# Optimization experiments

Hardware: AMD Instinct MI355X
Metric: run time of the kernel (lower is better)

The kernel has to match this reference:

```python
import math
import jax, jax.numpy as jnp
import numpy as np

DIM = 512
HEADS = 8
B, N = 4, 2048


def _linear_params(key, d_in, d_out):
    # torch nn.Linear default init: U(-1/sqrt(d_in), 1/sqrt(d_in))
    k1, k2 = jax.random.split(key)
    bound = 1.0 / math.sqrt(d_in)
    W = jax.random.uniform(k1, (d_out, d_in), minval=-bound, maxval=bound, dtype=jnp.float32)
    b = jax.random.uniform(k2, (d_out,), minval=-bound, maxval=bound, dtype=jnp.float32)
    return W, b


def setup_inputs() -> dict:
    key = jax.random.key(0)
    kq, kv, km, k1, k2, k3, k4 = jax.random.split(key, 7)
    Q = jax.random.normal(kq, (B, N, DIM), dtype=jnp.float32)
    V = jax.random.normal(kv, (B, N, DIM), dtype=jnp.float32)
    mask = jax.random.bernoulli(km, 0.9, (B, N))  # bool [B, Nk]
    Wq, bq = _linear_params(k1, DIM, DIM)
    Wk, bk = _linear_params(k2, DIM, DIM)
    Wv, bv = _linear_params(k3, DIM, DIM)
    Wo, bo = _linear_params(k4, DIM, DIM)
    return {"Q": Q, "V": V, "mask": mask,
            "Wq": Wq, "bq": bq, "Wk": Wk, "bk": bk,
            "Wv": Wv, "bv": bv, "Wo": Wo, "bo": bo}


def reference(Q, V, mask, Wq, bq, Wk, bk, Wv, bv, Wo, bo):
    Bb, Nq, _ = Q.shape
    dv = Wq.shape[0]
    h = HEADS
    d = dv // h
    q = Q @ Wq.T + bq          # [B, Nq, dv]
    k = V @ Wk.T + bk          # [B, Nk, dv]
    v = V @ Wv.T + bv          # [B, Nk, dv]
    # split heads: torch.cat(split(dim_split, dim=2), dim=0) == head-major stacking
    qh = q.reshape(Bb, Nq, h, d).transpose(2, 0, 1, 3)   # [h, B, Nq, d]
    kh = k.reshape(Bb, -1, h, d).transpose(2, 0, 1, 3)   # [h, B, Nk, d]
    vh = v.reshape(Bb, -1, h, d).transpose(2, 0, 1, 3)   # [h, B, Nk, d]
    # NOTE: original scales by sqrt(Q.shape[-1]) AFTER projection == sqrt(dim_V)
    logits = jnp.einsum('hbqd,hbkd->hbqk', qh, kh) / math.sqrt(dv)
    logits = jnp.where(mask[None, :, None, :], logits, jnp.float32(-100.0))
    A = jax.nn.softmax(logits, axis=-1)
    Oh = qh + jnp.einsum('hbqk,hbkd->hbqd', A, vh)       # residual inside attention
    O = Oh.transpose(1, 2, 0, 3).reshape(Bb, Nq, dv)     # merge heads
    return O + jax.nn.relu(O @ Wo.T + bo)
```

## Files before the change

kernel.cpp:

```cpp
#include <hip/hip_runtime.h>


typedef __attribute__((ext_vector_type(8))) __bf16 bf16x8;
typedef __attribute__((ext_vector_type(4))) float f32x4;

#define DEV static __device__ __forceinline__

constexpr int DIMC = 512;
constexpr int NTOK = 2048;
constexpr int BB   = 4;
constexpr int MTOK = BB * NTOK;
constexpr float SCALE2 = 0.04419417382415922f * 1.4426950408889634f;

DEV unsigned short f2b(float f) {
  unsigned u = __float_as_uint(f);
  u = (u + 0x7FFFu + ((u >> 16) & 1u)) >> 16;
  return (unsigned short)u;
}
DEV float b2f(unsigned short b) { return __uint_as_float(((unsigned)b) << 16); }

DEV unsigned cvtpk(float a, float b) {
  unsigned r;
  asm("v_cvt_pk_bf16_f32 %0, %1, %2" : "=v"(r) : "v"(a), "v"(b));
  return r;
}

DEV bf16x8 pack8(unsigned d0, unsigned d1, unsigned d2, unsigned d3) {
  union { unsigned u[4]; bf16x8 v; } t;
  t.u[0] = d0; t.u[1] = d1; t.u[2] = d2; t.u[3] = d3;
  return t.v;
}

DEV void async_cp16(const void* src, void* dst) {
  __builtin_amdgcn_global_load_lds(
      (const __attribute__((address_space(1))) void*)(src),
      (__attribute__((address_space(3))) void*)(dst), 16, 0, 0);
}

__global__ __launch_bounds__(256) void proj_gemm(
    const float* __restrict__ Qf, const float* __restrict__ Vf,
    const float* __restrict__ Wq, const float* __restrict__ Wk,
    const float* __restrict__ Wv,
    const float* __restrict__ bq, const float* __restrict__ bk,
    const float* __restrict__ bv,
    unsigned short* __restrict__ qbf, unsigned short* __restrict__ kbf,
    unsigned short* __restrict__ vtb,
    const unsigned char* __restrict__ mask, int* __restrict__ flag) {
  __shared__ union {
    struct { float A[2][4096]; float B[2][4096]; } s;
    unsigned short LT[128 * 136];
  } lds;

  const int region = blockIdx.z;
  const float* Af = (region == 0) ? Qf : Vf;
  const float* W = (region == 0) ? Wq : (region == 1) ? Wk : Wv;
  const float* bias = (region == 0) ? bq : (region == 1) ? bk : bv;

  const int tid = threadIdx.x;
  const int lane = tid & 63;
  const int w = tid >> 6;
  const int r = lane & 15, g = lane >> 4;
  const int rowB = blockIdx.x * 128;
  const int colB = blockIdx.y * 128;
  const int rw = (w >> 1) * 64, cw = (w & 1) * 64;

  if (region == 0 && blockIdx.x == 0 && blockIdx.y == 0) {
    int any = 0;
    for (int i = tid; i < BB * NTOK; i += 256)
      if ((i & 3) == 1 && mask[i]) any = 1;
    if (any) atomicOr(flag, 1);
  }

  auto stageT = [&](float* dst, const float* src, int kk) {
#pragma unroll
    for (int i = 0; i < 4; ++i) {
      int off = i * 4096 + tid * 16;
      int row = off >> 7;
      int c = ((off >> 4) & 7) ^ (row & 7);
      async_cp16(src + (size_t)row * DIMC + kk + c * 4, (char*)dst + off);
    }
  };

  f32x4 acc[4][4];
#pragma unroll
  for (int i = 0; i < 4; ++i)
#pragma unroll
    for (int j = 0; j < 4; ++j) acc[i][j] = f32x4{0.f, 0.f, 0.f, 0.f};

  stageT(lds.s.A[0], Af + (size_t)rowB * DIMC, 0);
  stageT(lds.s.B[0], W + (size_t)colB * DIMC, 0);
  __syncthreads();

  int cur = 0;
  for (int kk = 0; kk < DIMC; kk += 32) {
    if (kk + 32 < DIMC) {
      stageT(lds.s.A[cur ^ 1], Af + (size_t)rowB * DIMC, kk + 32);
      stageT(lds.s.B[cur ^ 1], W + (size_t)colB * DIMC, kk + 32);
    }
    const char* ap = (const char*)lds.s.A[cur];
    const char* bp = (const char*)lds.s.B[cur];
    bf16x8 af[4], bw[4];
#pragma unroll
    for (int i = 0; i < 4; ++i) {
      int row = rw + i * 16 + r;
      f32x4 lo = *reinterpret_cast<const f32x4*>(
          ap + row * 128 + (((2 * g) ^ (row & 7)) << 4));
      f32x4 hi = *reinterpret_cast<const f32x4*>(
          ap + row * 128 + (((2 * g + 1) ^ (row & 7)) << 4));
      af[i] = pack8(cvtpk(lo[0], lo[1]), cvtpk(lo[2], lo[3]),
                    cvtpk(hi[0], hi[1]), cvtpk(hi[2], hi[3]));
    }
#pragma unroll
    for (int j = 0; j < 4; ++j) {
      int row = cw + j * 16 + r;
      f32x4 lo = *reinterpret_cast<const f32x4*>(
          bp + row * 128 + (((2 * g) ^ (row & 7)) << 4));
      f32x4 hi = *reinterpret_cast<const f32x4*>(
          bp + row * 128 + (((2 * g + 1) ^ (row & 7)) << 4));
      bw[j] = pack8(cvtpk(lo[0], lo[1]), cvtpk(lo[2], lo[3]),
                    cvtpk(hi[0], hi[1]), cvtpk(hi[2], hi[3]));
    }
    __builtin_amdgcn_s_setprio(1);
#pragma unroll
    for (int i = 0; i < 4; ++i)
#pragma unroll
      for (int j = 0; j < 4; ++j)
        acc[i][j] = __builtin_amdgcn_mfma_f32_16x16x32_bf16(af[i], bw[j],
                                                            acc[i][j], 0, 0, 0);
    __builtin_amdgcn_s_setprio(0);
    __syncthreads();
    cur ^= 1;
  }

  if (region != 2) {
    const float sc = (region == 1) ? SCALE2 : 1.0f;
    unsigned short* dst = (region == 1) ? kbf : qbf;
#pragma unroll
    for (int i = 0; i < 4; ++i)
#pragma unroll
      for (int j = 0; j < 4; ++j) {
        int n = colB + cw + j * 16 + r;
        float bn = bias[n];
#pragma unroll
        for (int q = 0; q < 4; ++q) {
          int m = rowB + rw + i * 16 + g * 4 + q;
          dst[(size_t)m * DIMC + n] = f2b((acc[i][j][q] + bn) * sc);
        }
      }
  } else {
#pragma unroll
    for (int i = 0; i < 4; ++i)
#pragma unroll
      for (int j = 0; j < 4; ++j) {
        int nl = cw + j * 16 + r;
        float bn = bias[colB + nl];
        int tl = rw + i * 16 + g * 4;
        ushort4 o;
        o.x = f2b(acc[i][j][0] + bn);
        o.y = f2b(acc[i][j][1] + bn);
        o.z = f2b(acc[i][j][2] + bn);
        o.w = f2b(acc[i][j][3] + bn);
        *reinterpret_cast<ushort4*>(&lds.LT[nl * 136 + tl]) = o;
      }
    __syncthreads();
    int bidx = rowB >> 11, t0 = rowB & 2047;
#pragma unroll
    for (int rd = 0; rd < 8; ++rd) {
      int idx = rd * 256 + tid;
      int dv = idx >> 4, ch = idx & 15;
      int gdv = colB + dv, h = gdv >> 6, dd = gdv & 63;
      ushort4 v0 = *reinterpret_cast<const ushort4*>(&lds.LT[dv * 136 + ch * 8]);
      ushort4 v1 = *reinterpret_cast<const ushort4*>(&lds.LT[dv * 136 + ch * 8 + 4]);
      unsigned short* dst = vtb + (size_t)((bidx * 8 + h) * 64 + dd) * NTOK + t0 + ch * 8;
      reinterpret_cast<ushort4*>(dst)[0] = v0;
      reinterpret_cast<ushort4*>(dst)[1] = v1;
    }
  }
}

__global__ __launch_bounds__(256) void out_gemm(
    const unsigned short* __restrict__ Obf, const float* __restrict__ W,
    const float* __restrict__ bias, float* __restrict__ outf) {
  __shared__ struct { unsigned short A[2][2048]; float B[2][4096]; } lds;

  const int tid = threadIdx.x;
  const int lane = tid & 63;
  const int w = tid >> 6;
  const int r = lane & 15, g = lane >> 4;
  const int rowB = blockIdx.x * 64;
  const int colB = blockIdx.y * 128;
  const int rw = (w >> 1) * 32, cw = (w & 1) * 64;

  auto stageA = [&](unsigned short* dst, int kk) {
    int off = tid * 16;
    int row = off >> 6;
    int c = ((off >> 4) & 3) ^ (row & 3);
    async_cp16(Obf + (size_t)(rowB + row) * DIMC + kk + c * 8, (char*)dst + off);
  };
  auto stageB = [&](float* dst, int kk) {
#pragma unroll
    for (int i = 0; i < 4; ++i) {
      int off = i * 4096 + tid * 16;
      int row = off >> 7;
      int c = ((off >> 4) & 7) ^ (row & 7);
      async_cp16(W + (size_t)(colB + row) * DIMC + kk + c * 4, (char*)dst + off);
    }
  };

  f32x4 acc[2][4];
#pragma unroll
  for (int i = 0; i < 2; ++i)
#pragma unroll
    for (int j = 0; j < 4; ++j) acc[i][j] = f32x4{0.f, 0.f, 0.f, 0.f};

  stageA(lds.A[0], 0);
  stageB(lds.B[0], 0);
  __syncthreads();

  int cur = 0;
  for (int kk = 0; kk < DIMC; kk += 32) {
    if (kk + 32 < DIMC) {
      stageA(lds.A[cur ^ 1], kk + 32);
      stageB(lds.B[cur ^ 1], kk + 32);
    }
    const char* ap = (const char*)lds.A[cur];
    const char* bp = (const char*)lds.B[cur];
    bf16x8 af[2], bw[4];
#pragma unroll
    for (int i = 0; i < 2; ++i) {
      int row = rw + i * 16 + r;
      af[i] = *reinterpret_cast<const bf16x8*>(ap + row * 64 + ((g ^ (row & 3)) * 16));
    }
#pragma unroll
    for (int j = 0; j < 4; ++j) {
      int row = cw + j * 16 + r;
      f32x4 lo = *reinterpret_cast<const f32x4*>(
          bp + row * 128 + (((2 * g) ^ (row & 7)) << 4));
      f32x4 hi = *reinterpret_cast<const f32x4*>(
          bp + row * 128 + (((2 * g + 1) ^ (row & 7)) << 4));
      bw[j] = pack8(cvtpk(lo[0], lo[1]), cvtpk(lo[2], lo[3]),
                    cvtpk(hi[0], hi[1]), cvtpk(hi[2], hi[3]));
    }
    __builtin_amdgcn_s_setprio(1);
#pragma unroll
    for (int i = 0; i < 2; ++i)
#pragma unroll
      for (int j = 0; j < 4; ++j)
        acc[i][j] = __builtin_amdgcn_mfma_f32_16x16x32_bf16(af[i], bw[j],
                                                            acc[i][j], 0, 0, 0);
    __builtin_amdgcn_s_setprio(0);
    __syncthreads();
    cur ^= 1;
  }

#pragma unroll
  for (int i = 0; i < 2; ++i)
#pragma unroll
    for (int j = 0; j < 4; ++j) {
      int n = colB + cw + j * 16 + r;
      float bn = bias[n];
#pragma unroll
      for (int q = 0; q < 4; ++q) {
        int m = rowB + rw + i * 16 + g * 4 + q;
        float val = acc[i][j][q] + bn;
        outf[(size_t)m * DIMC + n] =
            b2f(Obf[(size_t)m * DIMC + n]) + fmaxf(val, 0.f);
      }
    }
}

__global__ __launch_bounds__(512, 4) void attn_kernel(
    const unsigned short* __restrict__ qb, const unsigned short* __restrict__ kb,
    const unsigned short* __restrict__ vt, const unsigned char* __restrict__ mask8,
    const int* __restrict__ flagp, unsigned short* __restrict__ Obf) {
  __shared__ unsigned short Kt[2][2][64 * 64];
  __shared__ unsigned short Vt[2][2][64 * 64];
  __shared__ float MaskAdd[NTOK];

  const int tid = threadIdx.x;
  const int lane = tid & 63;
  const int w = tid >> 6;
  const int kg = w >> 2;
  const int wq = w & 3;
  const int r = lane & 15, g = lane >> 4;
  const int bh = blockIdx.x, b = bh >> 3, h = bh & 7;
  const int q0 = blockIdx.y * 128 + wq * 32;
  const size_t rowbase = (size_t)b * NTOK;
  const int flag = *flagp;
  const unsigned* mask32 = (const unsigned*)mask8;

  for (int i = tid; i < NTOK; i += 512) {
    unsigned v = flag ? (unsigned)mask8[b * NTOK + i] : mask32[b * NTOK + i];
    MaskAdd[i] = v ? 0.f : -16384.f;
  }

  bf16x8 aq0[2], aq1[2];
#pragma unroll
  for (int ks = 0; ks < 2; ++ks) {
    aq0[ks] = *reinterpret_cast<const bf16x8*>(
        qb + (rowbase + q0 + r) * DIMC + h * 64 + ks * 32 + g * 8);
    aq1[ks] = *reinterpret_cast<const bf16x8*>(
        qb + (rowbase + q0 + 16 + r) * DIMC + h * 64 + ks * 32 + g * 8);
  }

  const unsigned short* kgb = kb + rowbase * DIMC + h * 64;
  const unsigned short* vgb = vt + (size_t)bh * 64 * NTOK;

  auto stageK = [&](int pb, int tile, int kt) {
    int off = tid * 16;
    int row = off >> 7;
    int s16 = ((off >> 4) & 7) ^ (row & 7);
    int ff = row >> 4, gg = (row >> 2) & 3, j = row & 3;
    int tok = 8 * gg + 4 * (ff & 1) + 32 * (ff >> 1) + j;
    async_cp16(kgb + (size_t)(kt + tok) * DIMC + (s16 << 3),
               (char*)&Kt[pb][tile][0] + off);
  };
  auto stageV = [&](int pb, int tile, int kt) {
    int off = tid * 16;
    int row = off >> 7;
    int s16 = ((off >> 4) & 7) ^ (row & 7);
    async_cp16(vgb + (size_t)row * NTOK + kt + (s16 << 3),
               (char*)&Vt[pb][tile][0] + off);
  };
  auto stagePair = [&](int pb, int p) {
    stageK(pb, 0, p * 128);
    stageK(pb, 1, p * 128 + 64);
    stageV(pb, 0, p * 128);
    stageV(pb, 1, p * 128 + 64);
  };

  stagePair(0, 0);
  __syncthreads();

  float lrun0 = 0.f, lrun1 = 0.f;
  f32x4 oacc0[4], oacc1[4];
#pragma unroll
  for (int f = 0; f < 4; ++f) {
    oacc0[f] = f32x4{0.f, 0.f, 0.f, 0.f};
    oacc1[f] = f32x4{0.f, 0.f, 0.f, 0.f};
  }

  const int swz = (r & 7) << 4;

  auto softmax_pa = [&](f32x4 (&s)[4], float& lr, bf16x8 (&pa)[2]) {
#pragma unroll
    for (int f = 0; f < 4; ++f)
#pragma unroll
      for (int j = 0; j < 4; ++j) s[f][j] = __builtin_exp2f(s[f][j]);
    float sf[4];
#pragma unroll
    for (int f = 0; f < 4; ++f)
      sf[f] = (s[f][0] + s[f][1]) + (s[f][2] + s[f][3]);
    lr += (sf[0] + sf[1]) + (sf[2] + sf[3]);
#pragma unroll
    for (int ks = 0; ks < 2; ++ks)
      pa[ks] = pack8(cvtpk(s[2 * ks][0], s[2 * ks][1]),
                     cvtpk(s[2 * ks][2], s[2 * ks][3]),
                     cvtpk(s[2 * ks + 1][0], s[2 * ks + 1][1]),
                     cvtpk(s[2 * ks + 1][2], s[2 * ks + 1][3]));
  };

  int cur = 0;
  for (int p = 0; p < NTOK / 128; ++p) {
    if (p + 1 < NTOK / 128) stagePair(cur ^ 1, p + 1);

    const int kt = p * 128 + kg * 64;

    f32x4 s0[4], s1[4];
#pragma unroll
    for (int f = 0; f < 4; ++f) {
      int tb = kt + 8 * g + 4 * (f & 1) + 32 * (f >> 1);
      f32x4 mc = *reinterpret_cast<const f32x4*>(&MaskAdd[tb]);
      s0[f] = mc;
      s1[f] = mc;
    }
    const unsigned char* kp = (const unsigned char*)&Kt[cur][kg][0];
    __builtin_amdgcn_s_setprio(1);
#pragma unroll
    for (int ks = 0; ks < 2; ++ks)
#pragma unroll
      for (int f = 0; f < 4; ++f) {
        bf16x8 kf = *reinterpret_cast<const bf16x8*>(
            kp + (f * 16 + r) * 128 + ((ks * 64 + g * 16) ^ swz));
        s0[f] = __builtin_amdgcn_mfma_f32_16x16x32_bf16(kf, aq0[ks], s0[f], 0, 0, 0);
        s1[f] = __builtin_amdgcn_mfma_f32_16x16x32_bf16(kf, aq1[ks], s1[f], 0, 0, 0);
      }
    __builtin_amdgcn_s_setprio(0);

    bf16x8 pa0[2], pa1[2];
    softmax_pa(s0, lrun0, pa0);
    softmax_pa(s1, lrun1, pa1);

    const unsigned char* vp = (const unsigned char*)&Vt[cur][kg][0];
    __builtin_amdgcn_s_setprio(1);
#pragma unroll
    for (int ks = 0; ks < 2; ++ks)
#pragma unroll
      for (int f = 0; f < 4; ++f) {
        bf16x8 vf = *reinterpret_cast<const bf16x8*>(
            vp + (f * 16 + r) * 128 + ((ks * 64 + g * 16) ^ swz));
        oacc0[f] = __builtin_amdgcn_mfma_f32_16x16x32_bf16(pa0[ks], vf, oacc0[f], 0, 0, 0);
        oacc1[f] = __builtin_amdgcn_mfma_f32_16x16x32_bf16(pa1[ks], vf, oacc1[f], 0, 0, 0);
      }
    __builtin_amdgcn_s_setprio(0);

    __syncthreads();
    cur ^= 1;
  }

  lrun0 += __shfl_xor(lrun0, 16);
  lrun0 += __shfl_xor(lrun0, 32);
  lrun1 += __shfl_xor(lrun1, 16);
  lrun1 += __shfl_xor(lrun1, 32);

  f32x4* cb4 = (f32x4*)&Kt[0][0][0];
  float* cl = (float*)&Vt[0][0][0];
  if (kg == 1) {
#pragma unroll
    for (int f = 0; f < 4; ++f) {
      cb4[wq * 512 + f * 64 + lane] = oacc0[f];
      cb4[wq * 512 + (4 + f) * 64 + lane] = oacc1[f];
    }
    if (g == 0) {
      cl[wq * 32 + r] = lrun0;
      cl[wq * 32 + 16 + r] = lrun1;
    }
  }
  __syncthreads();
  if (kg == 0) {
#pragma unroll
    for (int f = 0; f < 4; ++f) {
      oacc0[f] += cb4[wq * 512 + f * 64 + lane];
      oacc1[f] += cb4[wq * 512 + (4 + f) * 64 + lane];
    }
    lrun0 += cl[wq * 32 + r];
    lrun1 += cl[wq * 32 + 16 + r];

    auto epilogue = [&](float lr, f32x4 (&oa)[4], int qoff) {
#pragma unroll
      for (int j = 0; j < 4; ++j) {
        float linv = 1.0f / __shfl(lr, (lane & 48) | (g * 4 + j));
        int row = q0 + qoff + g * 4 + j;
#pragma unroll
        for (int f = 0; f < 4; ++f) {
          int col = h * 64 + f * 16 + r;
          size_t idx = (rowbase + row) * DIMC + col;
          Obf[idx] = f2b(b2f(qb[idx]) + oa[f][j] * linv);
        }
      }
    };
    epilogue(lrun0, oacc0, 0);
    epilogue(lrun1, oacc1, 16);
  }
}

extern "C" void kernel_launch(void* const* d_in, const int* in_sizes, int n_in,
                              void* d_out, int out_size, void* d_ws, size_t ws_size,
                              hipStream_t stream) {
  const float* Q  = (const float*)d_in[0];
  const float* V  = (const float*)d_in[1];
  const unsigned char* mask = (const unsigned char*)d_in[2];
  const float* Wq = (const float*)d_in[3];
  const float* bq = (const float*)d_in[4];
  const float* Wk = (const float*)d_in[5];
  const float* bk = (const float*)d_in[6];
  const float* Wv = (const float*)d_in[7];
  const float* bv = (const float*)d_in[8];
  const float* Wo = (const float*)d_in[9];
  const float* bo = (const float*)d_in[10];

  char* ws = (char*)d_ws;
  size_t off = 0;
  auto alloc = [&](size_t bytes) -> void* {
    void* p = ws + off;
    off += (bytes + 255) & ~(size_t)255;
    return p;
  };
  int* flag = (int*)alloc(4);
  unsigned short* qbf = (unsigned short*)alloc((size_t)MTOK * DIMC * 2);
  unsigned short* kbf = (unsigned short*)alloc((size_t)MTOK * DIMC * 2);
  unsigned short* vtb = (unsigned short*)alloc((size_t)MTOK * DIMC * 2);
  unsigned short* Obf = (unsigned short*)alloc((size_t)MTOK * DIMC * 2);

  hipMemsetAsync(flag, 0, 4, stream);

  proj_gemm<<<dim3(64, 4, 3), 256, 0, stream>>>(
      Q, V, Wq, Wk, Wv, bq, bk, bv, qbf, kbf, vtb, mask, flag);

  attn_kernel<<<dim3(BB * 8, NTOK / 128), 512, 0, stream>>>(
      qbf, kbf, vtb, mask, flag, Obf);

  out_gemm<<<dim3(128, 4), 256, 0, stream>>>(
      Obf, Wo, bo, (float*)d_out);
}
```

Measured before the change: 112.2 us.

## Fuse K and V projections into one block sharing the V activation tile

The projection kernel now runs two z-regions instead of three. Region 1 computes both the K and V projections in the same block, so each V activation tile is loaded from memory and converted to bf16 once for both. The K and V weights are prefetched into registers, converted to bf16 and written to LDS as packed bf16, which halves their LDS footprint and removes the per-fragment conversion. The cost is doubled accumulator registers (128 fp32 per thread) in the fused path, which may lower occupancy or cause spills, and fewer, heavier blocks.

```diff
diff --git a/kernel.cpp b/kernel.cpp
--- a/kernel.cpp
+++ b/kernel.cpp
@@ -47,15 +47,13 @@
     unsigned short* __restrict__ vtb,
     const unsigned char* __restrict__ mask, int* __restrict__ flag) {
   __shared__ union {
-    struct { float A[2][4096]; float B[2][4096]; } s;
+    struct { float A[2][4096]; float B[2][4096]; } q;
+    struct { float A[2][4096]; unsigned short Bk[2][4096];
+             unsigned short Bv[2][4096]; } kv;
     unsigned short LT[128 * 136];
   } lds;
 
   const int region = blockIdx.z;
-  const float* Af = (region == 0) ? Qf : Vf;
-  const float* W = (region == 0) ? Wq : (region == 1) ? Wk : Wv;
-  const float* bias = (region == 0) ? bq : (region == 1) ? bk : bv;
-
   const int tid = threadIdx.x;
   const int lane = tid & 63;
   const int w = tid >> 6;
@@ -80,101 +78,183 @@
       async_cp16(src + (size_t)row * DIMC + kk + c * 4, (char*)dst + off);
     }
   };
-
-  f32x4 acc[4][4];
+  auto loadAf = [&](const char* ap, int row) -> bf16x8 {
+    f32x4 lo = *reinterpret_cast<const f32x4*>(
+        ap + row * 128 + (((2 * g) ^ (row & 7)) << 4));
+    f32x4 hi = *reinterpret_cast<const f32x4*>(
+        ap + row * 128 + (((2 * g + 1) ^ (row & 7)) << 4));
+    return pack8(cvtpk(lo[0], lo[1]), cvtpk(lo[2], lo[3]),
+                 cvtpk(hi[0], hi[1]), cvtpk(hi[2], hi[3]));
+  };
+
+  if (region == 0) {
+    f32x4 acc[4][4];
+#pragma unroll
+    for (int i = 0; i < 4; ++i)
+#pragma unroll
+      for (int j = 0; j < 4; ++j) acc[i][j] = f32x4{0.f, 0.f, 0.f, 0.f};
+
+    stageT(lds.q.A[0], Qf + (size_t)rowB * DIMC, 0);
+    stageT(lds.q.B[0], Wq + (size_t)colB * DIMC, 0);
+    __syncthreads();
+
+    int cur = 0;
+    for (int kk = 0; kk < DIMC; kk += 32) {
+      if (kk + 32 < DIMC) {
+        stageT(lds.q.A[cur ^ 1], Qf + (size_t)rowB * DIMC, kk + 32);
+        stageT(lds.q.B[cur ^ 1], Wq + (size_t)colB * DIMC, kk + 32);
+      }
+      const char* ap = (const char*)lds.q.A[cur];
+      const char* bp = (const char*)lds.q.B[cur];
+      bf16x8 af[4], bw[4];
+#pragma unroll
+      for (int i = 0; i < 4; ++i) af[i] = loadAf(ap, rw + i * 16 + r);
+#pragma unroll
+      for (int j = 0; j < 4; ++j) bw[j] = loadAf(bp, cw + j * 16 + r);
+      __builtin_amdgcn_s_setprio(1);
+#pragma unroll
+      for (int i = 0; i < 4; ++i)
+#pragma unroll
+        for (int j = 0; j < 4; ++j)
+          acc[i][j] = __builtin_amdgcn_mfma_f32_16x16x32_bf16(af[i], bw[j],
+                                                              acc[i][j], 0, 0, 0);
+      __builtin_amdgcn_s_setprio(0);
+      __syncthreads();
+      cur ^= 1;
+    }
+
+#pragma unroll
+    for (int i = 0; i < 4; ++i)
+#pragma unroll
+      for (int j = 0; j < 4; ++j) {
+        int n = colB + cw + j * 16 + r;
+        float bn = bq[n];
+#pragma unroll
+        for (int q = 0; q < 4; ++q) {
+          int m = rowB + rw + i * 16 + g * 4 + q;
+          qbf[(size_t)m * DIMC + n] = f2b(acc[i][j][q] + bn);
+        }
+      }
+    return;
+  }
+
+  const int wrow = tid >> 1, whs = tid & 1;
+  f32x4 wkr[4], wvr[4];
+  auto loadW = [&](f32x4* dst, const float* W, int kk) {
+#pragma unroll
+    for (int sI = 0; sI < 2; ++sI) {
+      int s = 2 * whs + sI;
+      int c = s ^ (wrow & 3);
+      const float* src = W + (size_t)(colB + wrow) * DIMC + kk + c * 8;
+      dst[sI * 2]     = *reinterpret_cast<const f32x4*>(src);
+      dst[sI * 2 + 1] = *reinterpret_cast<const f32x4*>(src + 4);
+    }
+  };
+  auto writeW = [&](unsigned short* B, const f32x4* v) {
+#pragma unroll
+    for (int sI = 0; sI < 2; ++sI) {
+      const f32x4& lo = v[sI * 2];
+      const f32x4& hi = v[sI * 2 + 1];
+      uint4 pk = make_uint4(cvtpk(lo[0], lo[1]), cvtpk(lo[2], lo[3]),
+                            cvtpk(hi[0], hi[1]), cvtpk(hi[2], hi[3]));
+      *reinterpret_cast<uint4*>((char*)B + wrow * 64 + (2 * whs + sI) * 16) = pk;
+    }
+  };
+
+  f32x4 acck[4][4], accv[4][4];
 #pragma unroll
   for (int i = 0; i < 4; ++i)
 #pragma unroll
-    for (int j = 0; j < 4; ++j) acc[i][j] = f32x4{0.f, 0.f, 0.f, 0.f};
-
-  stageT(lds.s.A[0], Af + (size_t)rowB * DIMC, 0);
-  stageT(lds.s.B[0], W + (size_t)colB * DIMC, 0);
+    for (int j = 0; j < 4; ++j) {
+      acck[i][j] = f32x4{0.f, 0.f, 0.f, 0.f};
+      accv[i][j] = f32x4{0.f, 0.f, 0.f, 0.f};
+    }
+
+  stageT(lds.kv.A[0], Vf + (size_t)rowB * DIMC, 0);
+  loadW(wkr, Wk, 0);
+  loadW(wvr, Wv, 0);
+  writeW(lds.kv.Bk[0], wkr);
+  writeW(lds.kv.Bv[0], wvr);
   __syncthreads();
 
   int cur = 0;
   for (int kk = 0; kk < DIMC; kk += 32) {
-    if (kk + 32 < DIMC) {
-      stageT(lds.s.A[cur ^ 1], Af + (size_t)rowB * DIMC, kk + 32);
-      stageT(lds.s.B[cur ^ 1], W + (size_t)colB * DIMC, kk + 32);
-    }
-    const char* ap = (const char*)lds.s.A[cur];
-    const char* bp = (const char*)lds.s.B[cur];
-    bf16x8 af[4], bw[4];
-#pragma unroll
-    for (int i = 0; i < 4; ++i) {
-      int row = rw + i * 16 + r;
-      f32x4 lo = *reinterpret_cast<const f32x4*>(
-          ap + row * 128 + (((2 * g) ^ (row & 7)) << 4));
-      f32x4 hi = *reinterpret_cast<const f32x4*>(
-          ap + row * 128 + (((2 * g + 1) ^ (row & 7)) << 4));
-      af[i] = pack8(cvtpk(lo[0], lo[1]), cvtpk(lo[2], lo[3]),
-                    cvtpk(hi[0], hi[1]), cvtpk(hi[2], hi[3]));
-    }
+    const bool nxt = (kk + 32 < DIMC);
+    if (nxt) {
+      stageT(lds.kv.A[cur ^ 1], Vf + (size_t)rowB * DIMC, kk + 32);
+      loadW(wkr, Wk, kk + 32);
+      loadW(wvr, Wv, kk + 32);
+    }
+    const char* ap = (const char*)lds.kv.A[cur];
+    const char* bpk = (const char*)lds.kv.Bk[cur];
+    const char* bpv = (const char*)lds.kv.Bv[cur];
+    bf16x8 af[4], bwk[4], bwv[4];
+#pragma unroll
+    for (int i = 0; i < 4; ++i) af[i] = loadAf(ap, rw + i * 16 + r);
 #pragma unroll
     for (int j = 0; j < 4; ++j) {
       int row = cw + j * 16 + r;
-      f32x4 lo = *reinterpret_cast<const f32x4*>(
-          bp + row * 128 + (((2 * g) ^ (row & 7)) << 4));
-      f32x4 hi = *reinterpret_cast<const f32x4*>(
-          bp + row * 128 + (((2 * g + 1) ^ (row & 7)) << 4));
-      bw[j] = pack8(cvtpk(lo[0], lo[1]), cvtpk(lo[2], lo[3]),
-                    cvtpk(hi[0], hi[1]), cvtpk(hi[2], hi[3]));
+      bwk[j] = *reinterpret_cast<const bf16x8*>(bpk + row * 64 + ((g ^ (row & 3)) * 16));
+      bwv[j] = *reinterpret_cast<const bf16x8*>(bpv + row * 64 + ((g ^ (row & 3)) * 16));
     }
     __builtin_amdgcn_s_setprio(1);
 #pragma unroll
     for (int i = 0; i < 4; ++i)
 #pragma unroll
-      for (int j = 0; j < 4; ++j)
-        acc[i][j] = __builtin_amdgcn_mfma_f32_16x16x32_bf16(af[i], bw[j],
-                                                            acc[i][j], 0, 0, 0);
+      for (int j = 0; j < 4; ++j) {
+        acck[i][j] = __builtin_amdgcn_mfma_f32_16x16x32_bf16(af[i], bwk[j],
+                                                             acck[i][j], 0, 0, 0);
+        accv[i][j] = __builtin_amdgcn_mfma_f32_16x16x32_bf16(af[i], bwv[j],
+                                                             accv[i][j], 0, 0, 0);
+      }
     __builtin_amdgcn_s_setprio(0);
+    if (nxt) {
+      writeW(lds.kv.Bk[cur ^ 1], wkr);
+      writeW(lds.kv.Bv[cur ^ 1], wvr);
+    }
     __syncthreads();
     cur ^= 1;
   }
 
-  if (region != 2) {
-    const float sc = (region == 1) ? SCALE2 : 1.0f;
-    unsigned short* dst = (region == 1) ? kbf : qbf;
-#pragma unroll
-    for (int i = 0; i < 4; ++i)
-#pragma unroll
-      for (int j = 0; j < 4; ++j) {
-        int n = colB + cw + j * 16 + r;
-        float bn = bias[n];
-#pragma unroll
-        for (int q = 0; q < 4; ++q) {
-          int m = rowB + rw + i * 16 + g * 4 + q;
-          dst[(size_t)m * DIMC + n] = f2b((acc[i][j][q] + bn) * sc);
-        }
-      }
-  } else {
-#pragma unroll
-    for (int i = 0; i < 4; ++i)
-#pragma unroll
-      for (int j = 0; j < 4; ++j) {
-        int nl = cw + j * 16 + r;
-        float bn = bias[colB + nl];
-        int tl = rw + i * 16 + g * 4;
-        ushort4 o;
-        o.x = f2b(acc[i][j][0] + bn);
-        o.y = f2b(acc[i][j][1] + bn);
-        o.z = f2b(acc[i][j][2] + bn);
-        o.w = f2b(acc[i][j][3] + bn);
-        *reinterpret_cast<ushort4*>(&lds.LT[nl * 136 + tl]) = o;
-      }
-    __syncthreads();
-    int bidx = rowB >> 11, t0 = rowB & 2047;
-#pragma unroll
-    for (int rd = 0; rd < 8; ++rd) {
-      int idx = rd * 256 + tid;
-      int dv = idx >> 4, ch = idx & 15;
-      int gdv = colB + dv, h = gdv >> 6, dd = gdv & 63;
-      ushort4 v0 = *reinterpret_cast<const ushort4*>(&lds.LT[dv * 136 + ch * 8]);
-      ushort4 v1 = *reinterpret_cast<const ushort4*>(&lds.LT[dv * 136 + ch * 8 + 4]);
-      unsigned short* dst = vtb + (size_t)((bidx * 8 + h) * 64 + dd) * NTOK + t0 + ch * 8;
-      reinterpret_cast<ushort4*>(dst)[0] = v0;
-      reinterpret_cast<ushort4*>(dst)[1] = v1;
-    }
+#pragma unroll
+  for (int i = 0; i < 4; ++i)
+#pragma unroll
+    for (int j = 0; j < 4; ++j) {
+      int n = colB + cw + j * 16 + r;
+      float bn = bk[n];
+#pragma unroll
+      for (int q = 0; q < 4; ++q) {
+        int m = rowB + rw + i * 16 + g * 4 + q;
+        kbf[(size_t)m * DIMC + n] = f2b((acck[i][j][q] + bn) * SCALE2);
+      }
+    }
+  __syncthreads();
+#pragma unroll
+  for (int i = 0; i < 4; ++i)
+#pragma unroll
+    for (int j = 0; j < 4; ++j) {
+      int nl = cw + j * 16 + r;
+      float bn = bv[colB + nl];
+      int tl = rw + i * 16 + g * 4;
+      ushort4 o;
+      o.x = f2b(accv[i][j][0] + bn);
+      o.y = f2b(accv[i][j][1] + bn);
+      o.z = f2b(accv[i][j][2] + bn);
+      o.w = f2b(accv[i][j][3] + bn);
+      *reinterpret_cast<ushort4*>(&lds.LT[nl * 136 + tl]) = o;
+    }
+  __syncthreads();
+  int bidx = rowB >> 11, t0 = rowB & 2047;
+#pragma unroll
+  for (int rd = 0; rd < 8; ++rd) {
+    int idx = rd * 256 + tid;
+    int dv = idx >> 4, ch = idx & 15;
+    int gdv = colB + dv, h = gdv >> 6, dd = gdv & 63;
+    ushort4 v0 = *reinterpret_cast<const ushort4*>(&lds.LT[dv * 136 + ch * 8]);
+    ushort4 v1 = *reinterpret_cast<const ushort4*>(&lds.LT[dv * 136 + ch * 8 + 4]);
+    unsigned short* dst = vtb + (size_t)((bidx * 8 + h) * 64 + dd) * NTOK + t0 + ch * 8;
+    reinterpret_cast<ushort4*>(dst)[0] = v0;
+    reinterpret_cast<ushort4*>(dst)[1] = v1;
   }
 }
 
@@ -484,7 +564,7 @@
 
   hipMemsetAsync(flag, 0, 4, stream);
 
-  proj_gemm<<<dim3(64, 4, 3), 256, 0, stream>>>(
+  proj_gemm<<<dim3(64, 4, 2), 256, 0, stream>>>(
       Q, V, Wq, Wk, Wv, bq, bk, bv, qbf, kbf, vtb, mask, flag);
 
   attn_kernel<<<dim3(BB * 8, NTOK / 128), 512, 0, stream>>>(
```

New measurement: 120.5 us. +7.4%, slower.
